# Optimization experiments

Measured on AMD Instinct MI355X. Metric: run time of the kernel, lower is better.

Reference implementation:

```python
import jax, jax.numpy as jnp
import numpy as np

N_PATTERNS = 8192  # N: number of stored patterns (rows of Weights)
N_BITS = 4096      # n: pattern dimension (state length)


def setup_inputs() -> dict:
    key = jax.random.key(0)
    k1, k2, k3 = jax.random.split(key, 3)
    # Stored patterns (Weights) and initial state are +/-1 spins, as in a
    # discrete Hopfield / dense associative memory.
    weights = jnp.where(jax.random.normal(k1, (N_PATTERNS, N_BITS)) >= 0, 1.0, -1.0).astype(jnp.float32)
    state = jnp.where(jax.random.normal(k2, (N_BITS,)) >= 0, 1.0, -1.0).astype(jnp.float32)
    # Shuffled visit order (original uses random.shuffle on arange(n)).
    perm = jax.random.permutation(k3, N_BITS).astype(jnp.int32)
    return {"weights": weights, "state": state, "perm": perm}


def _energy_from_h(h):
    # energy(state) = -sum(F(W @ state, 2)) with F(x,2) = relu(x)**2
    return -jnp.sum(jnp.square(jnp.maximum(h, 0.0)))


def reference(weights, state, perm):
    # h = W @ state, maintained incrementally: flipping bit i changes h by
    # -2 * state[i] * W[:, i], which is exactly the same linear math as the
    # original full recompute per flip.
    h0 = weights @ state                      # [N]
    e0 = _energy_from_h(h0)

    def step(carry, i):
        h, vals, prev = carry
        col = jnp.take(weights, i, axis=1)    # W[:, i], gather of one column
        vi = vals[i]
        h_new = h - 2.0 * vi * col
        e_new = _energy_from_h(h_new)
        accept = e_new < prev                 # accept flip iff energy decreases
        h = jnp.where(accept, h_new, h)
        vals = vals.at[i].set(jnp.where(accept, -vi, vi))
        prev = jnp.where(accept, e_new, prev)
        return (h, vals, prev), None

    (_, vals, _), _ = jax.lax.scan(step, (h0, state, e0), perm)
    return vals
```

## Files before the change

kernel.cpp:

```cpp
#include <hip/hip_runtime.h>
#include <cstdint>

#define NPAT 8192
#define NBITS 4096

typedef float f32x2 __attribute__((ext_vector_type(2)));


__global__ void pack_kernel(const float* __restrict__ W, const float* __restrict__ state,
                            uint32_t* __restrict__ Bt) {
    int b = blockIdx.x & 63;
    int i = (blockIdx.x >> 6) * 256 + threadIdx.x;
    uint32_t spre = (__float_as_uint(state[i]) >> 31) ^ 1u;
    uint32_t wd0 = 0, wd1 = 0, wd2 = 0, wd3 = 0;
    const float* base = W + (size_t)(128 * b) * NBITS + i;
    #pragma unroll
    for (int q = 0; q < 128; ++q) {
        uint32_t bit = (__float_as_uint(base[(size_t)q * NBITS]) >> 31) ^ spre;
        int j = q & 7, k = q >> 3;
        int a = j >> 1, hi = j & 1;
        uint32_t add = bit << (16 * hi + k);
        if (a == 0) wd0 |= add;
        else if (a == 1) wd1 |= add;
        else if (a == 2) wd2 |= add;
        else wd3 |= add;
    }
    *(uint4*)(Bt + (size_t)i * 256 + 4 * b) = make_uint4(wd0, wd1, wd2, wd3);
}

__global__ void gemv_kernel(const float* __restrict__ W, const float* __restrict__ state,
                            float* __restrict__ h0) {
    int wid = threadIdx.x >> 6, lane = threadIdx.x & 63;
    int p = blockIdx.x * 4 + wid;
    const float* row = W + (size_t)p * NBITS;
    float acc = 0.f;
    for (int k = lane; k < NBITS; k += 64) acc += row[k] * state[k];
    #pragma unroll
    for (int d = 1; d < 64; d <<= 1) acc += __shfl_xor(acc, d, 64);
    if (lane == 0) h0[p] = acc;
}

__device__ __forceinline__ f32x2 pk_add(f32x2 a, f32x2 b) {
    f32x2 d;
    asm("v_pk_add_f32 %0, %1, %2" : "=v"(d) : "v"(a), "v"(b));
    return d;
}
__device__ __forceinline__ f32x2 pk_mul(f32x2 a, f32x2 b) {
    f32x2 d;
    asm("v_pk_mul_f32 %0, %1, %2" : "=v"(d) : "v"(a), "v"(b));
    return d;
}
__device__ __forceinline__ f32x2 pk_fma(f32x2 a, f32x2 b, f32x2 c) {
    f32x2 d;
    asm("v_pk_fma_f32 %0, %1, %2, %3" : "=v"(d) : "v"(a), "v"(b), "v"(c));
    return d;
}

__device__ __forceinline__ float tree_reduce(float x) {
    x = __uint_as_float(__builtin_amdgcn_update_dpp(__float_as_uint(x), __float_as_uint(x),
                                                    0xB1, 0xf, 0xf, false)) + x;
    x = __uint_as_float(__builtin_amdgcn_update_dpp(__float_as_uint(x), __float_as_uint(x),
                                                    0x4E, 0xf, 0xf, false)) + x;
    x = __uint_as_float(__builtin_amdgcn_update_dpp(__float_as_uint(x), __float_as_uint(x),
                                                    0x141, 0xf, 0xf, false)) + x;
    x = __uint_as_float(__builtin_amdgcn_update_dpp(__float_as_uint(x), __float_as_uint(x),
                                                    0x140, 0xf, 0xf, false)) + x;
#if __has_builtin(__builtin_amdgcn_permlane16_swap)
    {
        auto pr = __builtin_amdgcn_permlane16_swap(__float_as_uint(x), __float_as_uint(x),
                                                   false, false);
        x = __uint_as_float(pr[0]) + __uint_as_float(pr[1]);
    }
#else
    x = __int_as_float(__builtin_amdgcn_ds_swizzle(__float_as_int(x), 0x401F)) + x;
#endif
#if __has_builtin(__builtin_amdgcn_permlane32_swap)
    {
        auto pr = __builtin_amdgcn_permlane32_swap(__float_as_uint(x), __float_as_uint(x),
                                                   false, false);
        x = __uint_as_float(pr[0]) + __uint_as_float(pr[1]);
    }
#else
    x += __shfl_xor(x, 32, 64);
#endif
    return x;
}

__launch_bounds__(256, 1)
__global__ void seq_kernel(const uint32_t* __restrict__ Bt, const float* __restrict__ h0,
                           const float* __restrict__ state, const int* __restrict__ perm,
                           float* __restrict__ out) {
    __shared__ alignas(16) float part[2][4];
    __shared__ int2 pv[NBITS];

    const int t = threadIdx.x;
    const int b = t >> 2, a = t & 3;
    const int lane = t & 63, wid = t >> 6;

    for (int q = t; q < NBITS; q += 256) {
        int ii = perm[q];
        pv[q] = make_int2(ii, __float_as_int(state[ii]));
    }

    f32x2 h[16];
    #pragma unroll
    for (int k = 0; k < 16; ++k) h[k] = *(const f32x2*)(h0 + 128 * b + 2 * a + 8 * k);

    __syncthreads();

    int2 q0 = pv[0], q1 = pv[1], q2 = pv[2], q3 = pv[3], q4 = pv[4], q5 = pv[5];
    uint32_t wd0 = Bt[(size_t)q0.x * 256 + t];
    uint32_t wq[4];
    wq[1] = Bt[(size_t)q1.x * 256 + t];
    wq[2] = Bt[(size_t)q2.x * 256 + t];
    wq[3] = Bt[(size_t)q3.x * 256 + t];
    wq[0] = Bt[(size_t)q4.x * 256 + t];
    int2 pvB = q5;
    int2 pva[2];
    pva[0] = q0;

    f32x2 dq[2][16];
    #pragma unroll
    for (int k = 0; k < 16; ++k) {
        uint32_t lo = ((wd0 << (31 - k)) & 0x80000000u) | 0x40000000u;
        uint32_t hi = ((wd0 << (15 - k)) & 0x80000000u) | 0x40000000u;
        dq[0][k] = (f32x2){__uint_as_float(lo), __uint_as_float(hi)};
    }

    float Sprev;
    {
        f32x2 r;
        #pragma unroll
        for (int k = 0; k < 16; ++k) {
            f32x2 x = h[k];
            x.x = fmaxf(x.x, 0.f);
            x.y = fmaxf(x.y, 0.f);
            r = (k == 0) ? pk_mul(x, x) : pk_fma(x, x, r);
        }
        float red = tree_reduce(r.x + r.y);
        if (lane == 0) part[1][wid] = red;
        asm volatile("s_waitcnt lgkmcnt(0)\n\ts_barrier" ::: "memory");
        float4 pS = *(const float4*)(&part[1][0]);
        Sprev = (pS.x + pS.y) + (pS.z + pS.w);
    }

    for (int sb = 0; sb < NBITS; sb += 4) {
        #pragma unroll
        for (int u = 0; u < 4; ++u) {
            const int s = sb + u;

            f32x2 r;
            #pragma unroll
            for (int k = 0; k < 16; ++k) {
                f32x2 vv = pk_add(h[k], dq[u & 1][k]);
                vv.x = fmaxf(vv.x, 0.f);
                vv.y = fmaxf(vv.y, 0.f);
                r = (k == 0) ? pk_mul(vv, vv) : pk_fma(vv, vv, r);
            }
            float red = tree_reduce(r.x + r.y);
            if (lane == 0) part[u & 1][wid] = red;
            asm volatile("s_waitcnt lgkmcnt(0)\n\ts_barrier" ::: "memory");
            float4 pS = *(const float4*)(&part[u & 1][0]);

            uint32_t wNext = wq[(u + 1) & 3];
            #pragma unroll
            for (int k = 0; k < 16; ++k) {
                uint32_t lo = ((wNext << (31 - k)) & 0x80000000u) | 0x40000000u;
                uint32_t hi = ((wNext << (15 - k)) & 0x80000000u) | 0x40000000u;
                dq[(u + 1) & 1][k] = (f32x2){__uint_as_float(lo), __uint_as_float(hi)};
            }
            wq[(u + 1) & 3] = Bt[(size_t)pvB.x * 256 + t];
            pvB = pv[(s + 6 < NBITS) ? s + 6 : NBITS - 1];
            pva[(u + 1) & 1] = pv[(s + 1 < NBITS) ? s + 1 : NBITS - 1];

            float S = (pS.x + pS.y) + (pS.z + pS.w);
            bool acc = S > Sprev;
            Sprev = acc ? S : Sprev;
            f32x2 af2;
            af2.x = af2.y = acc ? 1.0f : 0.0f;
            int2 po = pva[u & 1];
            if (t == 0) {
                float vi = __int_as_float(po.y);
                out[po.x] = acc ? -vi : vi;
            }
            #pragma unroll
            for (int k = 0; k < 16; ++k) h[k] = pk_fma(dq[u & 1][k], af2, h[k]);
        }
    }
}

extern "C" void kernel_launch(void* const* d_in, const int* in_sizes, int n_in,
                              void* d_out, int out_size, void* d_ws, size_t ws_size,
                              hipStream_t stream) {
    const float* W     = (const float*)d_in[0];
    const float* state = (const float*)d_in[1];
    const int*   perm  = (const int*)d_in[2];
    float*       out   = (float*)d_out;

    uint32_t* Bt = (uint32_t*)d_ws;
    float*    h0 = (float*)((char*)d_ws + (size_t)4096 * 256 * 4);

    pack_kernel<<<1024, 256, 0, stream>>>(W, state, Bt);
    gemv_kernel<<<2048, 256, 0, stream>>>(W, state, h0);
    seq_kernel<<<1, 256, 0, stream>>>(Bt, h0, state, perm, out);
}
```

Measured before the change: 2.238 ms.

## Speculatively evaluate two flips per barrier by computing all three candidate energies

The sequential loop now handles two bits per iteration. It computes the energies for flipping bit a alone, bit b alone, and both bits, and then resolves both accept decisions from those three values. This halves the number of block-wide barriers and reductions on the serial critical path, at the cost of about 1.5x the arithmetic and three tree reductions per iteration. The prefetch distance for packed columns is adjusted to match, and the inline-asm packed ops are replaced with compiler builtins.

```diff
diff --git a/kernel.cpp b/kernel.cpp
--- a/kernel.cpp
+++ b/kernel.cpp
@@ -5,6 +5,7 @@
 #define NBITS 4096
 
 typedef float f32x2 __attribute__((ext_vector_type(2)));
+typedef unsigned int u32;
 
 
 __global__ void pack_kernel(const float* __restrict__ W, const float* __restrict__ state,
@@ -40,22 +41,6 @@
     if (lane == 0) h0[p] = acc;
 }
 
-__device__ __forceinline__ f32x2 pk_add(f32x2 a, f32x2 b) {
-    f32x2 d;
-    asm("v_pk_add_f32 %0, %1, %2" : "=v"(d) : "v"(a), "v"(b));
-    return d;
-}
-__device__ __forceinline__ f32x2 pk_mul(f32x2 a, f32x2 b) {
-    f32x2 d;
-    asm("v_pk_mul_f32 %0, %1, %2" : "=v"(d) : "v"(a), "v"(b));
-    return d;
-}
-__device__ __forceinline__ f32x2 pk_fma(f32x2 a, f32x2 b, f32x2 c) {
-    f32x2 d;
-    asm("v_pk_fma_f32 %0, %1, %2, %3" : "=v"(d) : "v"(a), "v"(b), "v"(c));
-    return d;
-}
-
 __device__ __forceinline__ float tree_reduce(float x) {
     x = __uint_as_float(__builtin_amdgcn_update_dpp(__float_as_uint(x), __float_as_uint(x),
                                                     0xB1, 0xf, 0xf, false)) + x;
@@ -86,11 +71,25 @@
     return x;
 }
 
+__device__ __forceinline__ f32x2 pkmax0(f32x2 v) {
+    f32x2 z = {0.0f, 0.0f};
+    return __builtin_elementwise_max(v, z);
+}
+
+#define GEN_D(dst, w)                                                       \
+    _Pragma("unroll")                                                       \
+    for (int k = 0; k < 16; ++k) {                                          \
+        u32 _lo = ((w << (31 - k)) & 0x80000000u) | 0x40000000u;            \
+        u32 _hi = ((w << (15 - k)) & 0x80000000u) | 0x40000000u;            \
+        dst[k] = (f32x2){__uint_as_float(_lo), __uint_as_float(_hi)};       \
+    }
+
 __launch_bounds__(256, 1)
 __global__ void seq_kernel(const uint32_t* __restrict__ Bt, const float* __restrict__ h0,
                            const float* __restrict__ state, const int* __restrict__ perm,
                            float* __restrict__ out) {
-    __shared__ alignas(16) float part[2][4];
+    __shared__ alignas(16) float part[2][3][4];
+    __shared__ alignas(16) float part0[4];
     __shared__ int2 pv[NBITS];
 
     const int t = threadIdx.x;
@@ -108,83 +107,102 @@
 
     __syncthreads();
 
-    int2 q0 = pv[0], q1 = pv[1], q2 = pv[2], q3 = pv[3], q4 = pv[4], q5 = pv[5];
-    uint32_t wd0 = Bt[(size_t)q0.x * 256 + t];
-    uint32_t wq[4];
-    wq[1] = Bt[(size_t)q1.x * 256 + t];
-    wq[2] = Bt[(size_t)q2.x * 256 + t];
-    wq[3] = Bt[(size_t)q3.x * 256 + t];
-    wq[0] = Bt[(size_t)q4.x * 256 + t];
-    int2 pvB = q5;
-    int2 pva[2];
-    pva[0] = q0;
-
-    f32x2 dq[2][16];
-    #pragma unroll
-    for (int k = 0; k < 16; ++k) {
-        uint32_t lo = ((wd0 << (31 - k)) & 0x80000000u) | 0x40000000u;
-        uint32_t hi = ((wd0 << (15 - k)) & 0x80000000u) | 0x40000000u;
-        dq[0][k] = (f32x2){__uint_as_float(lo), __uint_as_float(hi)};
-    }
+    u32 wA[4], wB[4];
+    #pragma unroll
+    for (int r = 0; r < 4; ++r) {
+        wA[r] = Bt[(size_t)pv[2 * r].x * 256 + t];
+        wB[r] = Bt[(size_t)pv[2 * r + 1].x * 256 + t];
+    }
+
+    f32x2 d0[2][16], d1[16];
+    GEN_D(d0[0], wA[0]);
+    GEN_D(d1, wB[0]);
 
     float Sprev;
     {
         f32x2 r;
         #pragma unroll
         for (int k = 0; k < 16; ++k) {
-            f32x2 x = h[k];
-            x.x = fmaxf(x.x, 0.f);
-            x.y = fmaxf(x.y, 0.f);
-            r = (k == 0) ? pk_mul(x, x) : pk_fma(x, x, r);
+            f32x2 x = pkmax0(h[k]);
+            r = (k == 0) ? x * x : __builtin_elementwise_fma(x, x, r);
         }
         float red = tree_reduce(r.x + r.y);
-        if (lane == 0) part[1][wid] = red;
+        if (lane == 0) part0[wid] = red;
         asm volatile("s_waitcnt lgkmcnt(0)\n\ts_barrier" ::: "memory");
-        float4 pS = *(const float4*)(&part[1][0]);
-        Sprev = (pS.x + pS.y) + (pS.z + pS.w);
-    }
-
-    for (int sb = 0; sb < NBITS; sb += 4) {
+        float4 p = *(const float4*)(&part0[0]);
+        Sprev = (p.x + p.y) + (p.z + p.w);
+    }
+
+    for (int rb = 0; rb < NBITS / 2; rb += 4) {
         #pragma unroll
         for (int u = 0; u < 4; ++u) {
-            const int s = sb + u;
-
-            f32x2 r;
+            const int rr = rb + u;
+            const int s  = 2 * rr;
+            const int pb = rr & 1;
+            const int cu = u & 1;
+
+            int2 pvi0 = pv[s];
+            int2 pvi1 = pv[s + 1];
+
+            f32x2 ra, rbv, rc;
             #pragma unroll
             for (int k = 0; k < 16; ++k) {
-                f32x2 vv = pk_add(h[k], dq[u & 1][k]);
-                vv.x = fmaxf(vv.x, 0.f);
-                vv.y = fmaxf(vv.y, 0.f);
-                r = (k == 0) ? pk_mul(vv, vv) : pk_fma(vv, vv, r);
-            }
-            float red = tree_reduce(r.x + r.y);
-            if (lane == 0) part[u & 1][wid] = red;
+                f32x2 va = h[k] + d0[cu][k];
+                f32x2 vb = h[k] + d1[k];
+                f32x2 vc = va + d1[k];
+                f32x2 xa = pkmax0(va), xb = pkmax0(vb), xc = pkmax0(vc);
+                if (k == 0) { ra = xa * xa; rbv = xb * xb; rc = xc * xc; }
+                else {
+                    ra  = __builtin_elementwise_fma(xa, xa, ra);
+                    rbv = __builtin_elementwise_fma(xb, xb, rbv);
+                    rc  = __builtin_elementwise_fma(xc, xc, rc);
+                }
+            }
+            float Ra = tree_reduce(ra.x + ra.y);
+            float Rb = tree_reduce(rbv.x + rbv.y);
+            float Rc = tree_reduce(rc.x + rc.y);
+            if (lane == 0) {
+                part[pb][0][wid] = Ra;
+                part[pb][1][wid] = Rb;
+                part[pb][2][wid] = Rc;
+            }
             asm volatile("s_waitcnt lgkmcnt(0)\n\ts_barrier" ::: "memory");
-            float4 pS = *(const float4*)(&part[u & 1][0]);
-
-            uint32_t wNext = wq[(u + 1) & 3];
+
+            GEN_D(d0[cu ^ 1], wA[(u + 1) & 3]);
+            int li0 = s + 8 < NBITS ? s + 8 : NBITS - 1;
+            int li1 = s + 9 < NBITS ? s + 9 : NBITS - 1;
+            int iA = pv[li0].x, iB = pv[li1].x;
+
+            float4 pa = *(const float4*)(&part[pb][0][0]);
+            float4 pq = *(const float4*)(&part[pb][1][0]);
+            float4 pc = *(const float4*)(&part[pb][2][0]);
+
+            wA[u] = Bt[(size_t)iA * 256 + t];
+            wB[u] = Bt[(size_t)iB * 256 + t];
+
+            float Sa = (pa.x + pa.y) + (pa.z + pa.w);
+            float Sb = (pq.x + pq.y) + (pq.z + pq.w);
+            float Sc = (pc.x + pc.y) + (pc.z + pc.w);
+
+            bool acc0 = Sa > Sprev;
+            bool acc1 = acc0 ? (Sc > Sa) : (Sb > Sprev);
+            Sprev = acc1 ? (acc0 ? Sc : Sb) : (acc0 ? Sa : Sprev);
+
+            if (t == 0) {
+                float v0 = __int_as_float(pvi0.y), v1 = __int_as_float(pvi1.y);
+                out[pvi0.x] = acc0 ? -v0 : v0;
+                out[pvi1.x] = acc1 ? -v1 : v1;
+            }
+
+            float f0s = acc0 ? 1.0f : 0.0f, f1s = acc1 ? 1.0f : 0.0f;
+            f32x2 f0 = {f0s, f0s}, f1 = {f1s, f1s};
             #pragma unroll
             for (int k = 0; k < 16; ++k) {
-                uint32_t lo = ((wNext << (31 - k)) & 0x80000000u) | 0x40000000u;
-                uint32_t hi = ((wNext << (15 - k)) & 0x80000000u) | 0x40000000u;
-                dq[(u + 1) & 1][k] = (f32x2){__uint_as_float(lo), __uint_as_float(hi)};
-            }
-            wq[(u + 1) & 3] = Bt[(size_t)pvB.x * 256 + t];
-            pvB = pv[(s + 6 < NBITS) ? s + 6 : NBITS - 1];
-            pva[(u + 1) & 1] = pv[(s + 1 < NBITS) ? s + 1 : NBITS - 1];
-
-            float S = (pS.x + pS.y) + (pS.z + pS.w);
-            bool acc = S > Sprev;
-            Sprev = acc ? S : Sprev;
-            f32x2 af2;
-            af2.x = af2.y = acc ? 1.0f : 0.0f;
-            int2 po = pva[u & 1];
-            if (t == 0) {
-                float vi = __int_as_float(po.y);
-                out[po.x] = acc ? -vi : vi;
-            }
-            #pragma unroll
-            for (int k = 0; k < 16; ++k) h[k] = pk_fma(dq[u & 1][k], af2, h[k]);
+                f32x2 hh = __builtin_elementwise_fma(d0[cu][k], f0, h[k]);
+                h[k] = __builtin_elementwise_fma(d1[k], f1, hh);
+            }
+
+            GEN_D(d1, wB[(u + 1) & 3]);
         }
     }
 }
```

After: 2.085 ms, median of 2. -6.8%, faster.
